# Performance work log

Hardware: AMD Instinct MI355X
Metric: run time of the kernel (lower is better)

## Reference

```python
import jax, jax.numpy as jnp
import numpy as np

B, S = 64, 64
IMG_F, EMB, HID, VOCAB = 2048, 512, 512, 32000


def setup_inputs() -> dict:
    key = jax.random.key(0)
    ks = jax.random.split(key, 12)
    s = 0.02
    return {
        "img": jax.random.normal(ks[0], (B, IMG_F), jnp.float32),
        "captions": jax.random.randint(ks[1], (B, S), 0, VOCAB),
        "embed_W": jax.random.normal(ks[2], (VOCAB, EMB), jnp.float32) * s,
        "Wi": jax.random.normal(ks[3], (IMG_F, HID), jnp.float32) * s,
        "bi": jax.random.normal(ks[4], (HID,), jnp.float32) * s,
        "Wx": jax.random.normal(ks[5], (EMB, HID), jnp.float32) * s,
        "bx": jax.random.normal(ks[6], (HID,), jnp.float32) * s,
        "Wh": jax.random.normal(ks[7], (HID, HID), jnp.float32) * s,
        "bh": jax.random.normal(ks[8], (HID, HID)[:1] + (HID,), jnp.float32)[0] * s if False else jax.random.normal(ks[8], (HID,), jnp.float32) * s,
        "Wy": jax.random.normal(ks[9], (HID, VOCAB), jnp.float32) * s,
        "by": jax.random.normal(ks[10], (VOCAB,), jnp.float32) * s,
    }


def reference(img, captions, embed_W, Wi, bi, Wx, bx, Wh, bh, Wy, by):
    # Embed caption inputs (drop last token): (B, T, EMB), T = S-1
    x = embed_W[captions[:, :-1]]
    # Precompute input-to-hidden preactivations for all steps: (B, T, HID)
    pre = jnp.einsum("bte,eh->bth", x, Wx) + bx
    # Image features are injected only at t=0 (as in the torch loop)
    pre = pre.at[:, 0].add(img @ Wi + bi)

    def step(h_prev, p_t):
        h_t = jnp.tanh(p_t + h_prev @ Wh + bh)
        return h_t, h_t

    h0 = jnp.zeros((img.shape[0], Wh.shape[0]), dtype=x.dtype)
    _, hs = jax.lax.scan(step, h0, pre.transpose(1, 0, 2))  # (T, B, HID)
    hs = hs.transpose(1, 0, 2)  # (B, T, HID)
    # Output projection in one big GEMM (same math as per-step h2y)
    logits = jnp.einsum("bth,hv->btv", hs, Wy) + by  # (B, T, VOCAB)
    return logits
```

## Files before the change

### kernel.cpp

```cpp
#include <hip/hip_runtime.h>
#include <hip/hip_bf16.h>

#define B_    64
#define S_    64
#define T_    63
#define IMGF  2048
#define EMB   512
#define HID   512
#define VOCAB 32000
#define MROWS 4032
#define MPAD  4096

typedef __bf16 bf16;
typedef __bf16 bf16x8 __attribute__((ext_vector_type(8)));
typedef float  f32x4  __attribute__((ext_vector_type(4)));

__device__ __forceinline__ void gload_lds16(const void* g, void* l) {
  __builtin_amdgcn_global_load_lds(
      (const __attribute__((address_space(1))) unsigned int*)g,
      (__attribute__((address_space(3))) unsigned int*)l, 16, 0, 0);
}

#define LGKM_BARRIER() asm volatile("s_waitcnt lgkmcnt(0)\n\ts_barrier" ::: "memory")

__global__ __launch_bounds__(256) void transpose_w(
    const float* __restrict__ W, bf16* __restrict__ WT, int K, int N)
{
  __shared__ float tile[64][65];
  const int tx = threadIdx.x & 63, ty = threadIdx.x >> 6;
  const int n0 = blockIdx.x * 64, k0 = blockIdx.y * 64;
  #pragma unroll
  for (int r = ty; r < 64; r += 4)
    tile[r][tx] = W[(size_t)(k0 + r) * N + n0 + tx];
  __syncthreads();
  #pragma unroll
  for (int r = ty; r < 64; r += 4)
    WT[(size_t)(n0 + r) * K + k0 + tx] = (bf16)tile[tx][r];
}

__global__ __launch_bounds__(256) void embed_gather(
    const float* __restrict__ embW, const int* __restrict__ captions,
    bf16* __restrict__ X)
{
  const int r = blockIdx.x;
  const int tid = threadIdx.x;
  if (r < MROWS) {
    const int b = r / T_, t = r % T_;
    const int idx = captions[b * S_ + t];
    float2 v = ((const float2*)(embW + (size_t)idx * EMB))[tid];
    X[(size_t)r * EMB + 2 * tid]     = (bf16)v.x;
    X[(size_t)r * EMB + 2 * tid + 1] = (bf16)v.y;
  } else {
    X[(size_t)r * EMB + 2 * tid]     = (bf16)0.f;
    X[(size_t)r * EMB + 2 * tid + 1] = (bf16)0.f;
  }
}

__global__ __launch_bounds__(256) void img_to_bf16(
    const float* __restrict__ img, bf16* __restrict__ imgB)
{
  const int r = blockIdx.x;
  const int tid = threadIdx.x;
  #pragma unroll
  for (int j = 0; j < 8; j++) {
    const int c = tid + j * 256;
    const float v = (r < B_) ? img[(size_t)r * IMGF + c] : 0.f;
    imgB[(size_t)r * IMGF + c] = (bf16)v;
  }
}

__global__ __launch_bounds__(256) void gemm_bt(
    const bf16* __restrict__ A, const bf16* __restrict__ BT,
    const float* __restrict__ bias, float* __restrict__ C,
    int Mvalid, int N, int K)
{
  __shared__ __align__(16) bf16 As[2][128 * 32];
  __shared__ __align__(16) bf16 Bs[2][128 * 32];
  const int tid  = threadIdx.x;
  const int wave = tid >> 6, lane = tid & 63;
  const int wm = wave >> 1, wn = wave & 1;
  const int bm = blockIdx.x, bn = blockIdx.y;
  const int lg = lane >> 4, lr = lane & 15;

  f32x4 acc[4][4];
  #pragma unroll
  for (int m = 0; m < 4; m++)
    #pragma unroll
    for (int n = 0; n < 4; n++) acc[m][n] = (f32x4){0.f, 0.f, 0.f, 0.f};

  const bf16* Abase = A  + (size_t)bm * 128 * K;
  const bf16* Bbase = BT + (size_t)bn * 128 * K;

  const int c0 = wave * 64 + lane;
  const int r0 = c0 >> 2,  sl0 = (c0 & 3) ^ ((r0 >> 1) & 3);
  const int c1 = 256 + c0;
  const int r1 = c1 >> 2,  sl1 = (c1 & 3) ^ ((r1 >> 1) & 3);

  const int NT = K >> 5;

#define STAGE_TILE(buf, kt)                                                   \
  do {                                                                        \
    gload_lds16(Abase + (size_t)r0 * K + (kt) + sl0 * 8,                      \
                &As[buf][(wave * 64) * 8]);                                   \
    gload_lds16(Abase + (size_t)r1 * K + (kt) + sl1 * 8,                      \
                &As[buf][(256 + wave * 64) * 8]);                             \
    gload_lds16(Bbase + (size_t)r0 * K + (kt) + sl0 * 8,                      \
                &Bs[buf][(wave * 64) * 8]);                                   \
    gload_lds16(Bbase + (size_t)r1 * K + (kt) + sl1 * 8,                      \
                &Bs[buf][(256 + wave * 64) * 8]);                             \
  } while (0)

  STAGE_TILE(0, 0);
  int cur = 0;
  for (int it = 0; it < NT; ++it) {
    __syncthreads();
    if (it + 1 < NT) STAGE_TILE(cur ^ 1, (it + 1) * 32);

    bf16x8 af[4], bfr[4];
    #pragma unroll
    for (int m = 0; m < 4; m++) {
      const int r = wm * 64 + m * 16 + lr;
      const int sp = lg ^ ((r >> 1) & 3);
      af[m] = *(const bf16x8*)&As[cur][r * 32 + sp * 8];
    }
    #pragma unroll
    for (int n = 0; n < 4; n++) {
      const int r = wn * 64 + n * 16 + lr;
      const int sp = lg ^ ((r >> 1) & 3);
      bfr[n] = *(const bf16x8*)&Bs[cur][r * 32 + sp * 8];
    }
    #pragma unroll
    for (int m = 0; m < 4; m++)
      #pragma unroll
      for (int n = 0; n < 4; n++)
        acc[m][n] = __builtin_amdgcn_mfma_f32_16x16x32_bf16(af[m], bfr[n], acc[m][n], 0, 0, 0);
    cur ^= 1;
  }
#undef STAGE_TILE

  const int row0 = bm * 128 + wm * 64 + (lane >> 4) * 4;
  const int col0 = bn * 128 + wn * 64 + lr;
  #pragma unroll
  for (int m = 0; m < 4; m++) {
    #pragma unroll
    for (int n = 0; n < 4; n++) {
      const int col = col0 + n * 16;
      const float bv = bias[col];
      #pragma unroll
      for (int q = 0; q < 4; q++) {
        const int row = row0 + m * 16 + q;
        if (row < Mvalid) C[(size_t)row * N + col] = acc[m][n][q] + bv;
      }
    }
  }
}

__global__ __launch_bounds__(512, 1) void gemm_bt256(
    const bf16* __restrict__ A, const bf16* __restrict__ BT,
    const float* __restrict__ bias, float* __restrict__ C,
    int Mvalid, int N, int K)
{
  __shared__ __align__(16) bf16 sm[4][2][256 * 32];
  const int tid  = threadIdx.x;
  const int wave = tid >> 6, lane = tid & 63;
  const int wm = wave >> 2, wn = wave & 3;
  const int bm = blockIdx.x, bn = blockIdx.y;
  const int lg = lane >> 4, lr = lane & 15;

  f32x4 acc[8][4];
  #pragma unroll
  for (int m = 0; m < 8; m++)
    #pragma unroll
    for (int n = 0; n < 4; n++) acc[m][n] = (f32x4){0.f, 0.f, 0.f, 0.f};

  const bf16* Abase = A  + (size_t)bm * 256 * K;
  const bf16* Bbase = BT + (size_t)bn * 256 * K;

  const int ca0 = tid,        ra0 = ca0 >> 2, sa0 = (ca0 & 3) ^ (ra0 & 3);
  const int ca1 = tid + 512,  ra1 = ca1 >> 2, sa1 = (ca1 & 3) ^ (ra1 & 3);
  const int ldsb0 = (wave * 64) * 8;
  const int ldsb1 = (512 + wave * 64) * 8;

#define STAGE256(buf, kt)                                                     \
  do {                                                                        \
    gload_lds16(Abase + (size_t)ra0 * K + (kt) + sa0 * 8, &sm[buf][0][ldsb0]);\
    gload_lds16(Abase + (size_t)ra1 * K + (kt) + sa1 * 8, &sm[buf][0][ldsb1]);\
    gload_lds16(Bbase + (size_t)ra0 * K + (kt) + sa0 * 8, &sm[buf][1][ldsb0]);\
    gload_lds16(Bbase + (size_t)ra1 * K + (kt) + sa1 * 8, &sm[buf][1][ldsb1]);\
  } while (0)

  const int NT = K >> 5;
  STAGE256(0, 0);
  STAGE256(1, 32);
  STAGE256(2, 64);

  #pragma unroll 1
  for (int it = 0; it < NT; ++it) {
    const int newer = (NT - 1 - it) > 2 ? 2 : (NT - 1 - it);
    switch (newer) {
      case 2:  asm volatile("s_waitcnt vmcnt(8)\n\ts_barrier" ::: "memory"); break;
      case 1:  asm volatile("s_waitcnt vmcnt(4)\n\ts_barrier" ::: "memory"); break;
      default: asm volatile("s_waitcnt vmcnt(0)\n\ts_barrier" ::: "memory"); break;
    }

    const bf16* As_ = sm[it & 3][0];
    const bf16* Bs_ = sm[it & 3][1];
    bf16x8 af[8], bfr[4];
    #pragma unroll
    for (int m = 0; m < 8; m++) {
      const int r = wm * 128 + m * 16 + lr;
      const int sp = lg ^ (r & 3);
      af[m] = *(const bf16x8*)&As_[(r * 4 + sp) * 8];
    }
    #pragma unroll
    for (int n = 0; n < 4; n++) {
      const int r = wn * 64 + n * 16 + lr;
      const int sp = lg ^ (r & 3);
      bfr[n] = *(const bf16x8*)&Bs_[(r * 4 + sp) * 8];
    }
    #pragma unroll
    for (int m = 0; m < 8; m++)
      #pragma unroll
      for (int n = 0; n < 4; n++)
        acc[m][n] = __builtin_amdgcn_mfma_f32_16x16x32_bf16(af[m], bfr[n], acc[m][n], 0, 0, 0);

    LGKM_BARRIER();
    if (it + 3 < NT) STAGE256((it + 3) & 3, (it + 3) * 32);
  }
#undef STAGE256

  const int row0 = bm * 256 + wm * 128 + lg * 4;
  const int col0 = bn * 256 + wn * 64 + lr;
  #pragma unroll
  for (int m = 0; m < 8; m++) {
    #pragma unroll
    for (int n = 0; n < 4; n++) {
      const int col = col0 + n * 16;
      const float bv = bias[col];
      #pragma unroll
      for (int q = 0; q < 4; q++) {
        const int row = row0 + m * 16 + q;
        if (row < Mvalid) C[(size_t)row * N + col] = acc[m][n][q] + bv;
      }
    }
  }
}

#define FREG 48
#define FLDS 16
__global__ __launch_bounds__(512, 1) void rnn_reg8(
    const float* __restrict__ pre, const bf16* __restrict__ WhT,
    const float* __restrict__ bh, const float* __restrict__ pimg,
    bf16* __restrict__ hs)
{
  const int bg  = blockIdx.x;
  const int tid = threadIdx.x;
  const int wave = tid >> 6, lane = tid & 63;
  const int lg = lane >> 4, lr = lane & 15;
  const int gb0 = bg * 16;
  const int wc0 = wave * 64;

  __shared__ __align__(16) bf16 hsh[16 * 512];
  __shared__ __align__(16) bf16 bls[8 * FLDS * 64 * 8];

  bf16x8 bw[FREG];
  #pragma unroll
  for (int f = 0; f < 64; f++) {
    const int n = f >> 4, kf = f & 15;
    const bf16x8 v = *(const bf16x8*)(WhT + (size_t)(wc0 + n * 16 + lr) * 512
                                          + kf * 32 + lg * 8);
    if (f < FREG) bw[f] = v;
    else *(bf16x8*)&bls[((wave * FLDS + (f - FREG)) * 64 + lane) * 8] = v;
  }

  *(f32x4*)&hsh[tid * 16]     = (f32x4){0.f, 0.f, 0.f, 0.f};
  *(f32x4*)&hsh[tid * 16 + 8] = (f32x4){0.f, 0.f, 0.f, 0.f};

  float bhv[4];
  #pragma unroll
  for (int n = 0; n < 4; n++) bhv[n] = bh[wc0 + n * 16 + lr];
  const float* preb = pre + ((size_t)(gb0 + lg * 4) * T_) * 512 + wc0 + lr;

  __syncthreads();

  #pragma unroll 1
  for (int t = 0; t < T_; t++) {
    float prq[4][4];
    #pragma unroll
    for (int n = 0; n < 4; n++)
      #pragma unroll
      for (int q = 0; q < 4; q++)
        prq[n][q] = preb[(size_t)q * (T_ * 512) + (size_t)t * 512 + n * 16];

    f32x4 acc[4];
    #pragma unroll
    for (int n = 0; n < 4; n++) acc[n] = (f32x4){0.f, 0.f, 0.f, 0.f};

    #pragma unroll
    for (int kf = 0; kf < 16; kf++) {
      const int c = (kf * 4 + lg) ^ (lr & 7);
      const bf16x8 a = *(const bf16x8*)&hsh[(lr * 64 + c) * 8];
      #pragma unroll
      for (int n = 0; n < 4; n++) {
        const int f = n * 16 + kf;
        bf16x8 bfrag;
        if (f < FREG) bfrag = bw[f];
        else bfrag = *(const bf16x8*)&bls[((wave * FLDS + (f - FREG)) * 64 + lane) * 8];
        acc[n] = __builtin_amdgcn_mfma_f32_16x16x32_bf16(a, bfrag, acc[n], 0, 0, 0);
      }
    }
    LGKM_BARRIER();

    #pragma unroll
    for (int n = 0; n < 4; n++) {
      #pragma unroll
      for (int q = 0; q < 4; q++) {
        const int bl = lg * 4 + q;
        const int b  = gb0 + bl;
        const int k  = wc0 + n * 16 + lr;
        float s = acc[n][q] + prq[n][q] + bhv[n];
        if (t == 0) s += pimg[(size_t)b * HID + k];
        const float e = __builtin_exp2f(s * 2.885390081777927f);
        const float hv = 1.f - 2.f * __builtin_amdgcn_rcpf(e + 1.f);
        hs[((size_t)b * T_ + t) * HID + k] = (bf16)hv;
        const int c = (k >> 3) ^ (bl & 7);
        hsh[bl * 512 + c * 8 + (k & 7)] = (bf16)hv;
      }
    }
    LGKM_BARRIER();
  }
}

extern "C" void kernel_launch(void* const* d_in, const int* in_sizes, int n_in,
                              void* d_out, int out_size, void* d_ws, size_t ws_size,
                              hipStream_t stream) {
  const float* img      = (const float*)d_in[0];
  const int*   captions = (const int*)d_in[1];
  const float* embW     = (const float*)d_in[2];
  const float* Wi       = (const float*)d_in[3];
  const float* bi       = (const float*)d_in[4];
  const float* Wx       = (const float*)d_in[5];
  const float* bx       = (const float*)d_in[6];
  const float* Wh       = (const float*)d_in[7];
  const float* bh       = (const float*)d_in[8];
  const float* Wy       = (const float*)d_in[9];
  const float* by       = (const float*)d_in[10];
  float* logits = (float*)d_out;

  char* ws = (char*)d_ws;
  bf16*  WyT  = (bf16*)(ws);
  bf16*  WxT  = (bf16*)(ws + 32768000);
  bf16*  X    = (bf16*)(ws + 33292288);
  bf16*  hs   = (bf16*)(ws + 37486592);
  float* pre  = (float*)(ws + 41680896);
  float* pimg = (float*)(ws + 49938432);
  bf16*  imgB = (bf16*)(ws + 50200576);
  bf16*  WiT  = (bf16*)(ws + 50724864);
  bf16*  WhT  = WxT;

  transpose_w<<<dim3(VOCAB / 64, HID / 64), 256, 0, stream>>>(Wy, WyT, HID, VOCAB);
  transpose_w<<<dim3(HID / 64, EMB / 64), 256, 0, stream>>>(Wx, WxT, EMB, HID);
  transpose_w<<<dim3(HID / 64, IMGF / 64), 256, 0, stream>>>(Wi, WiT, IMGF, HID);
  img_to_bf16<<<128, 256, 0, stream>>>(img, imgB);

  embed_gather<<<MPAD, 256, 0, stream>>>(embW, captions, X);

  gemm_bt<<<dim3(MPAD / 128, HID / 128), 256, 0, stream>>>(X, WxT, bx, pre, MROWS, HID, HID);

  gemm_bt<<<dim3(1, HID / 128), 256, 0, stream>>>(imgB, WiT, bi, pimg, B_, HID, IMGF);

  transpose_w<<<dim3(HID / 64, HID / 64), 256, 0, stream>>>(Wh, WhT, HID, HID);

  hipMemsetAsync(hs + (size_t)MROWS * HID, 0,
                 (size_t)(MPAD - MROWS) * HID * sizeof(bf16), stream);

  rnn_reg8<<<4, 512, 0, stream>>>(pre, WhT, bh, pimg, hs);

  gemm_bt256<<<dim3(MPAD / 256, VOCAB / 256), 512, 0, stream>>>(hs, WyT, by, logits, MROWS, VOCAB, HID);
}
```

Before: 646.4 us.

## Pre-tile Wy into swizzled LDS layout and remap GEMM blocks for L2 locality

The Wy transpose kernel now writes a blocked layout: per 256-column tile and 32-wide k slice, data sits contiguously with the LDS swizzle already applied. The output GEMM can then stage B with fully contiguous 16-byte loads. The swizzle pattern changes from (r&3) to ((r>>1)&3) to cut LDS bank conflicts. The grid becomes 1D with an XCD-aware block remap so neighbouring blocks share B tiles in cache. The cost is a more complex scatter in the transpose and hardcoded tile counts (bm & 15) in the GEMM.

```diff
diff --git a/kernel.cpp b/kernel.cpp
--- a/kernel.cpp
+++ b/kernel.cpp
@@ -36,6 +36,27 @@
   #pragma unroll
   for (int r = ty; r < 64; r += 4)
     WT[(size_t)(n0 + r) * K + k0 + tx] = (bf16)tile[tx][r];
+}
+
+__global__ __launch_bounds__(256) void transpose_wy_tiled(
+    const float* __restrict__ W, bf16* __restrict__ T)
+{
+  __shared__ float tile[64][65];
+  const int tx = threadIdx.x & 63, ty = threadIdx.x >> 6;
+  const int n0 = blockIdx.x * 64, k0 = blockIdx.y * 64;
+  #pragma unroll
+  for (int r = ty; r < 64; r += 4)
+    tile[r][tx] = W[(size_t)(k0 + r) * VOCAB + n0 + tx];
+  __syncthreads();
+  #pragma unroll
+  for (int r = ty; r < 64; r += 4) {
+    const int n = n0 + r, k = k0 + tx;
+    const int bn = n >> 8, rr = n & 255, kt = k >> 5;
+    const int sl = ((k & 31) >> 3) ^ ((rr >> 1) & 3);
+    const size_t dst = (((size_t)(bn * 16 + kt) * 1024 + rr * 4 + sl) << 3)
+                     + (k & 7);
+    T[dst] = (bf16)tile[tx][r];
+  }
 }
 
 __global__ __launch_bounds__(256) void embed_gather(
@@ -156,7 +177,7 @@
 }
 
 __global__ __launch_bounds__(512, 1) void gemm_bt256(
-    const bf16* __restrict__ A, const bf16* __restrict__ BT,
+    const bf16* __restrict__ A, const bf16* __restrict__ Btile,
     const float* __restrict__ bias, float* __restrict__ C,
     int Mvalid, int N, int K)
 {
@@ -164,35 +185,41 @@
   const int tid  = threadIdx.x;
   const int wave = tid >> 6, lane = tid & 63;
   const int wm = wave >> 2, wn = wave & 3;
-  const int bm = blockIdx.x, bn = blockIdx.y;
   const int lg = lane >> 4, lr = lane & 15;
 
+  const int id  = blockIdx.x;
+  const int cpx = gridDim.x >> 3;
+  const int swz = (id & 7) * cpx + (id >> 3);
+  const int bm  = swz & 15, bn = swz >> 4;
+
   f32x4 acc[8][4];
   #pragma unroll
   for (int m = 0; m < 8; m++)
     #pragma unroll
     for (int n = 0; n < 4; n++) acc[m][n] = (f32x4){0.f, 0.f, 0.f, 0.f};
 
-  const bf16* Abase = A  + (size_t)bm * 256 * K;
-  const bf16* Bbase = BT + (size_t)bn * 256 * K;
-
-  const int ca0 = tid,        ra0 = ca0 >> 2, sa0 = (ca0 & 3) ^ (ra0 & 3);
-  const int ca1 = tid + 512,  ra1 = ca1 >> 2, sa1 = (ca1 & 3) ^ (ra1 & 3);
+  const bf16* Abase = A + (size_t)bm * 256 * K;
+
+  const int ca0 = tid,        ra0 = ca0 >> 2, sa0 = (ca0 & 3) ^ ((ra0 >> 1) & 3);
+  const int ca1 = tid + 512,  ra1 = ca1 >> 2, sa1 = (ca1 & 3) ^ ((ra1 >> 1) & 3);
   const int ldsb0 = (wave * 64) * 8;
   const int ldsb1 = (512 + wave * 64) * 8;
 
-#define STAGE256(buf, kt)                                                     \
+#define STAGE256(buf, kti)                                                    \
   do {                                                                        \
-    gload_lds16(Abase + (size_t)ra0 * K + (kt) + sa0 * 8, &sm[buf][0][ldsb0]);\
-    gload_lds16(Abase + (size_t)ra1 * K + (kt) + sa1 * 8, &sm[buf][0][ldsb1]);\
-    gload_lds16(Bbase + (size_t)ra0 * K + (kt) + sa0 * 8, &sm[buf][1][ldsb0]);\
-    gload_lds16(Bbase + (size_t)ra1 * K + (kt) + sa1 * 8, &sm[buf][1][ldsb1]);\
+    const bf16* Bt_ = Btile + (((size_t)bn * 16 + (kti)) << 13);              \
+    gload_lds16(Abase + (size_t)ra0 * K + (kti) * 32 + sa0 * 8,               \
+                &sm[buf][0][ldsb0]);                                          \
+    gload_lds16(Abase + (size_t)ra1 * K + (kti) * 32 + sa1 * 8,               \
+                &sm[buf][0][ldsb1]);                                          \
+    gload_lds16(Bt_ + (size_t)tid * 8,         &sm[buf][1][ldsb0]);           \
+    gload_lds16(Bt_ + (size_t)(tid + 512) * 8, &sm[buf][1][ldsb1]);           \
   } while (0)
 
   const int NT = K >> 5;
   STAGE256(0, 0);
-  STAGE256(1, 32);
-  STAGE256(2, 64);
+  STAGE256(1, 1);
+  STAGE256(2, 2);
 
   #pragma unroll 1
   for (int it = 0; it < NT; ++it) {
@@ -209,13 +236,13 @@
     #pragma unroll
     for (int m = 0; m < 8; m++) {
       const int r = wm * 128 + m * 16 + lr;
-      const int sp = lg ^ (r & 3);
+      const int sp = lg ^ ((r >> 1) & 3);
       af[m] = *(const bf16x8*)&As_[(r * 4 + sp) * 8];
     }
     #pragma unroll
     for (int n = 0; n < 4; n++) {
       const int r = wn * 64 + n * 16 + lr;
-      const int sp = lg ^ (r & 3);
+      const int sp = lg ^ ((r >> 1) & 3);
       bfr[n] = *(const bf16x8*)&Bs_[(r * 4 + sp) * 8];
     }
     #pragma unroll
@@ -225,7 +252,7 @@
         acc[m][n] = __builtin_amdgcn_mfma_f32_16x16x32_bf16(af[m], bfr[n], acc[m][n], 0, 0, 0);
 
     LGKM_BARRIER();
-    if (it + 3 < NT) STAGE256((it + 3) & 3, (it + 3) * 32);
+    if (it + 3 < NT) STAGE256((it + 3) & 3, it + 3);
   }
 #undef STAGE256
 
@@ -358,7 +385,7 @@
   bf16*  WiT  = (bf16*)(ws + 50724864);
   bf16*  WhT  = WxT;
 
-  transpose_w<<<dim3(VOCAB / 64, HID / 64), 256, 0, stream>>>(Wy, WyT, HID, VOCAB);
+  transpose_wy_tiled<<<dim3(VOCAB / 64, HID / 64), 256, 0, stream>>>(Wy, WyT);
   transpose_w<<<dim3(HID / 64, EMB / 64), 256, 0, stream>>>(Wx, WxT, EMB, HID);
   transpose_w<<<dim3(HID / 64, IMGF / 64), 256, 0, stream>>>(Wi, WiT, IMGF, HID);
   img_to_bf16<<<128, 256, 0, stream>>>(img, imgB);
@@ -376,5 +403,6 @@
 
   rnn_reg8<<<4, 512, 0, stream>>>(pre, WhT, bh, pimg, hs);
 
-  gemm_bt256<<<dim3(MPAD / 256, VOCAB / 256), 512, 0, stream>>>(hs, WyT, by, logits, MROWS, VOCAB, HID);
-}
+  gemm_bt256<<<(MPAD / 256) * (VOCAB / 256), 512, 0, stream>>>(
+      hs, WyT, by, logits, MROWS, VOCAB, HID);
+}
```

Result: no change. 637.9 us (-1.3%).
